# Kernel optimization log

Hardware: AMD Instinct MI355X
Metric: run time of the kernel (lower is better)

The kernel has to match this reference:

```python
import jax, jax.numpy as jnp
import numpy as np

B, N, C = 4, 2048, 64   # batch, tokens, num_feat
HS = 512                # hidden_size
H = HS // C             # 8 heads, head_dim = C = 64
EPS = 1e-6


def _ln(x, g, b):
    m = x.mean(-1, keepdims=True)
    v = ((x - m) ** 2).mean(-1, keepdims=True)
    return (x - m) / jnp.sqrt(v + EPS) * g + b


def setup_inputs() -> dict:
    key = jax.random.key(0)
    ks = jax.random.split(key, 8)
    s = 0.02
    return {
        "x": jax.random.normal(ks[0], (B, N, C), jnp.float32),
        "g1": jnp.ones((C,), jnp.float32),
        "be1": jnp.zeros((C,), jnp.float32),
        "Wqkv": jax.random.normal(ks[1], (C, 3 * HS), jnp.float32) * s,
        "bqkv": jnp.zeros((3 * HS,), jnp.float32),
        "Wout": jax.random.normal(ks[2], (HS, C), jnp.float32) * s,
        "bout": jnp.zeros((C,), jnp.float32),
        "g2": jnp.ones((C,), jnp.float32),
        "be2": jnp.zeros((C,), jnp.float32),
        "W1": jax.random.normal(ks[3], (C, HS // 8), jnp.float32) * s,
        "b1": jax.random.normal(ks[4], (HS // 8,), jnp.float32) * 1e-6,
        "W2": jax.random.normal(ks[5], (HS // 8, C), jnp.float32) * s,
        "b2": jax.random.normal(ks[6], (C,), jnp.float32) * 1e-6,
    }


def reference(x, g1, be1, Wqkv, bqkv, Wout, bout, g2, be2, W1, b1, W2, b2):
    b_, n_, c_ = x.shape
    hs = Wout.shape[0]
    h_ = hs // c_
    res = x
    y = _ln(x, g1, be1)
    # fused QKV: (B,N,3*HS) -> (3,B,H,N,D) with D = c_
    qkv = (y @ Wqkv + bqkv).reshape(b_, n_, 3, h_, c_).transpose(2, 0, 3, 1, 4)
    q, k, v = qkv[0], qkv[1], qkv[2]
    scores = jnp.einsum('bhqd,bhkd->bhqk', q, k) / jnp.sqrt(jnp.asarray(c_, x.dtype))
    probs = jax.nn.softmax(scores, axis=-1)
    ctx = jnp.einsum('bhqk,bhkd->bhqd', probs, v)
    ctx = ctx.transpose(0, 2, 1, 3).reshape(b_, n_, hs)
    attn = jax.nn.gelu(ctx @ Wout + bout, approximate=False)  # GELU after out proj per source
    x2 = attn + res
    y2 = _ln(x2, g2, be2)
    mlp = jax.nn.gelu(y2 @ W1 + b1, approximate=False) @ W2 + b2
    return mlp + x2
```

## Files before the change

### kernel.cpp

```cpp
#include <hip/hip_runtime.h>


#define NN 2048
#define CC 64
#define HH 8
#define HSZ 512

typedef __bf16 bf16x8 __attribute__((ext_vector_type(8)));
typedef float f32x4 __attribute__((ext_vector_type(4)));

__device__ __forceinline__ float b2f(unsigned short u) {
  union { unsigned int i; float f; } v; v.i = ((unsigned int)u) << 16; return v.f;
}
__device__ __forceinline__ unsigned short f2b(float f) {
  union { float f; unsigned int i; } v; v.f = f;
  unsigned int r = v.i + 0x7FFFu + ((v.i >> 16) & 1u);
  return (unsigned short)(r >> 16);
}
__device__ __forceinline__ unsigned int pk2(float a, float b) {
  return (unsigned int)f2b(a) | ((unsigned int)f2b(b) << 16);
}
__device__ __forceinline__ unsigned char f2fp8(float f) {
  int p = __builtin_amdgcn_cvt_pk_fp8_f32(f, f, 0, false);
  return (unsigned char)(p & 0xFF);
}
__device__ __forceinline__ float gelu_f(float x) {
  return 0.5f * x * (1.0f + erff(x * 0.7071067811865475f));
}

__global__ __launch_bounds__(256) void k_ln_qkv(
    const float* __restrict__ x,
    const float* __restrict__ g1,
    const float* __restrict__ be1,
    const float* __restrict__ W,
    const float* __restrict__ bqkv,
    unsigned char* __restrict__ Qb,
    unsigned char* __restrict__ Kb,
    unsigned char* __restrict__ VbT)
{
  __shared__ __align__(16) unsigned short As[64 * 72];
  __shared__ __align__(16) unsigned short Ws[128 * 72];
  const int tid = threadIdx.x, wv = tid >> 6, lane = tid & 63;
  const int col = lane & 15, quad = lane >> 4;
  const int bm = blockIdx.x & 127, bn = blockIdx.x >> 7;
  const int m0 = bm * 64, nw = bn * 128;

  const int c4 = tid & 15;
  float4 gv = *(const float4*)(g1 + c4 * 4);
  float4 bv = *(const float4*)(be1 + c4 * 4);
  #pragma unroll
  for (int s = 0; s < 4; ++s) {
    int idx = s * 256 + tid;
    int row = idx >> 4;
    float4 xv = *(const float4*)(x + (size_t)(m0 + row) * CC + c4 * 4);
    float ps = xv.x + xv.y + xv.z + xv.w;
    float ps2 = xv.x * xv.x + xv.y * xv.y + xv.z * xv.z + xv.w * xv.w;
    #pragma unroll
    for (int off = 8; off; off >>= 1) {
      ps += __shfl_xor(ps, off, 16);
      ps2 += __shfl_xor(ps2, off, 16);
    }
    float mean = ps * (1.0f / 64.0f);
    float var = ps2 * (1.0f / 64.0f) - mean * mean;
    float rs = rsqrtf(var + 1e-6f);
    uint2 packed;
    packed.x = pk2((xv.x - mean) * rs * gv.x + bv.x, (xv.y - mean) * rs * gv.y + bv.y);
    packed.y = pk2((xv.z - mean) * rs * gv.z + bv.z, (xv.w - mean) * rs * gv.w + bv.w);
    *(uint2*)&As[row * 72 + c4 * 4] = packed;
  }

  {
    const int c_loc = tid & 127;
    const int kg = tid >> 7;
    const int ng = nw + c_loc;
    #pragma unroll
    for (int g = 0; g < 4; ++g) {
      float wv8[8];
      #pragma unroll
      for (int j = 0; j < 8; ++j) wv8[j] = W[(size_t)(kg * 32 + g * 8 + j) * 1536 + ng];
      uint4 u;
      u.x = pk2(wv8[0], wv8[1]); u.y = pk2(wv8[2], wv8[3]);
      u.z = pk2(wv8[4], wv8[5]); u.w = pk2(wv8[6], wv8[7]);
      *(uint4*)&Ws[c_loc * 72 + kg * 32 + g * 8] = u;
    }
  }
  __syncthreads();

  bf16x8 af0 = *(const bf16x8*)&As[(wv * 16 + col) * 72 + quad * 8];
  bf16x8 af1 = *(const bf16x8*)&As[(wv * 16 + col) * 72 + 32 + quad * 8];

  f32x4 acc[8];
  #pragma unroll
  for (int nt = 0; nt < 8; ++nt) acc[nt] = (f32x4){0.f, 0.f, 0.f, 0.f};
  #pragma unroll
  for (int nt = 0; nt < 8; ++nt) {
    bf16x8 b0 = *(const bf16x8*)&Ws[(nt * 16 + col) * 72 + quad * 8];
    bf16x8 b1 = *(const bf16x8*)&Ws[(nt * 16 + col) * 72 + 32 + quad * 8];
    acc[nt] = __builtin_amdgcn_mfma_f32_16x16x32_bf16(af0, b0, acc[nt], 0, 0, 0);
    acc[nt] = __builtin_amdgcn_mfma_f32_16x16x32_bf16(af1, b1, acc[nt], 0, 0, 0);
  }

  const int tkb = m0 + wv * 16 + quad * 4;
  const int bb = tkb >> 11;
  const int nnb = tkb & 2047;
  #pragma unroll
  for (int nt = 0; nt < 8; ++nt) {
    const int n0 = nw + nt * 16;
    const int which = n0 >> 9;
    const int h = (n0 >> 6) & 7;
    const int d0 = n0 & 63;
    const float bias = bqkv[n0 + col];
    float vv[4];
    #pragma unroll
    for (int r = 0; r < 4; ++r) vv[r] = acc[nt][r] + bias;
    if (which == 2) {
      int lo = __builtin_amdgcn_cvt_pk_fp8_f32(vv[0], vv[1], 0, false);
      int full = __builtin_amdgcn_cvt_pk_fp8_f32(vv[2], vv[3], lo, true);
      *(unsigned int*)(VbT + ((size_t)(bb * HH + h) * CC + d0 + col) * NN + nnb) =
          (unsigned int)full;
    } else {
      unsigned char* dst = (which == 0) ? Qb : Kb;
      #pragma unroll
      for (int r = 0; r < 4; ++r)
        dst[((size_t)(bb * HH + h) * NN + nnb + r) * CC + d0 + col] = f2fp8(vv[r]);
    }
  }
}

__global__ __launch_bounds__(256) void k_attn(
    const unsigned char* __restrict__ Q,
    const unsigned char* __restrict__ K,
    const unsigned char* __restrict__ VT,
    const float* __restrict__ Wout,
    unsigned short* __restrict__ part)
{
  __shared__ __align__(16) unsigned char smem[18432];
  unsigned char* Ks = smem;
  unsigned char* Vt = smem + 5120;
  unsigned char* Ps = smem + 10240;
  unsigned short* Wb = (unsigned short*)smem;
  unsigned short* Ob = (unsigned short*)(smem + 9216);
  const int tid = threadIdx.x, wv = tid >> 6, lane = tid & 63;
  const int col = lane & 15, quad = lane >> 4;
  const int bh = blockIdx.x >> 5, qc = blockIdx.x & 31;
  const size_t base = (size_t)bh * NN * CC;
  const int q0 = qc * 64 + wv * 16;

  long qf0 = *(const long*)(Q + base + (size_t)(q0 + col) * CC + quad * 8);
  long qf1 = *(const long*)(Q + base + (size_t)(q0 + col) * CC + 32 + quad * 8);

  f32x4 o[4];
  float lsum[4] = {0.f, 0.f, 0.f, 0.f};
  #pragma unroll
  for (int dt = 0; dt < 4; ++dt) o[dt] = (f32x4){0.f, 0.f, 0.f, 0.f};
  unsigned char* Pw = Ps + wv * (16 * 80);

  for (int kt = 0; kt < 32; ++kt) {
    const int kb = kt * 64;
    {
      int row = tid >> 2, c16 = (tid & 3) << 4;
      *(uint4*)&Ks[row * 80 + c16] = *(const uint4*)(K + base + (size_t)(kb + row) * CC + c16);
      *(uint4*)&Vt[row * 80 + c16] = *(const uint4*)(VT + base + (size_t)row * NN + kb + c16);
    }
    __syncthreads();

    #pragma unroll
    for (int ct = 0; ct < 4; ++ct) {
      long k0 = *(const long*)&Ks[(ct * 16 + col) * 80 + quad * 8];
      long k1 = *(const long*)&Ks[(ct * 16 + col) * 80 + 32 + quad * 8];
      f32x4 a = (f32x4){0.f, 0.f, 0.f, 0.f};
      a = __builtin_amdgcn_mfma_f32_16x16x32_fp8_fp8(qf0, k0, a, 0, 0, 0);
      a = __builtin_amdgcn_mfma_f32_16x16x32_fp8_fp8(qf1, k1, a, 0, 0, 0);
      #pragma unroll
      for (int r = 0; r < 4; ++r) {
        float pv = __expf(a[r] * 0.125f);
        lsum[r] += pv;
        Pw[(quad * 4 + r) * 80 + ct * 16 + col] = f2fp8(pv);
      }
    }
    long pa0 = *(const long*)&Pw[col * 80 + quad * 8];
    long pa1 = *(const long*)&Pw[col * 80 + 32 + quad * 8];
    #pragma unroll
    for (int dt = 0; dt < 4; ++dt) {
      long v0 = *(const long*)&Vt[(dt * 16 + col) * 80 + quad * 8];
      long v1 = *(const long*)&Vt[(dt * 16 + col) * 80 + 32 + quad * 8];
      o[dt] = __builtin_amdgcn_mfma_f32_16x16x32_fp8_fp8(pa0, v0, o[dt], 0, 0, 0);
      o[dt] = __builtin_amdgcn_mfma_f32_16x16x32_fp8_fp8(pa1, v1, o[dt], 0, 0, 0);
    }
    __syncthreads();
  }

  #pragma unroll
  for (int r = 0; r < 4; ++r) {
    float v = lsum[r];
    #pragma unroll
    for (int off = 8; off; off >>= 1) v += __shfl_xor(v, off, 16);
    float inv = 1.0f / v;
    #pragma unroll
    for (int dt = 0; dt < 4; ++dt) o[dt][r] *= inv;
  }

  const int h = bh & 7, b = bh >> 3;
  {
    const int c = tid & 63, kg = tid >> 6;
    #pragma unroll
    for (int j = 0; j < 16; ++j)
      Wb[c * 72 + kg * 16 + j] = f2b(Wout[(size_t)(h * 64 + kg * 16 + j) * 64 + c]);
  }
  unsigned short* Obw = Ob + wv * (16 * 72);
  #pragma unroll
  for (int dt = 0; dt < 4; ++dt)
    #pragma unroll
    for (int r = 0; r < 4; ++r)
      Obw[(quad * 4 + r) * 72 + dt * 16 + col] = f2b(o[dt][r]);
  __syncthreads();

  bf16x8 oa0 = *(const bf16x8*)&Obw[col * 72 + quad * 8];
  bf16x8 oa1 = *(const bf16x8*)&Obw[col * 72 + 32 + quad * 8];
  #pragma unroll
  for (int nt = 0; nt < 4; ++nt) {
    bf16x8 bw0 = *(const bf16x8*)&Wb[(nt * 16 + col) * 72 + quad * 8];
    bf16x8 bw1 = *(const bf16x8*)&Wb[(nt * 16 + col) * 72 + 32 + quad * 8];
    f32x4 ac = (f32x4){0.f, 0.f, 0.f, 0.f};
    ac = __builtin_amdgcn_mfma_f32_16x16x32_bf16(oa0, bw0, ac, 0, 0, 0);
    ac = __builtin_amdgcn_mfma_f32_16x16x32_bf16(oa1, bw1, ac, 0, 0, 0);
    #pragma unroll
    for (int r = 0; r < 4; ++r) {
      int n = q0 + quad * 4 + r;
      part[((size_t)(b * HH + h) * NN + n) * CC + nt * 16 + col] = f2b(ac[r]);
    }
  }
}

__global__ __launch_bounds__(256) void k_post(
    const unsigned short* __restrict__ part,
    const float* __restrict__ x,
    const float* __restrict__ bout,
    const float* __restrict__ g2,
    const float* __restrict__ be2,
    const float* __restrict__ W1,
    const float* __restrict__ b1,
    const float* __restrict__ W2,
    const float* __restrict__ b2v,
    float* __restrict__ out)
{
  __shared__ __align__(16) float Ws1[64 * 64];
  __shared__ __align__(16) float Ws2[64 * 64];
  __shared__ float ys[4][64], hs[4][64];
  const int tid = threadIdx.x, wid = tid >> 6, lane = tid & 63;
  const int tk = blockIdx.x * 4 + wid;
  const int b = tk >> 11, n = tk & 2047;

  #pragma unroll
  for (int p = 0; p < 4; ++p) {
    int idx = p * 256 + tid;
    *(float4*)&Ws1[idx * 4] = *(const float4*)(W1 + idx * 4);
    *(float4*)&Ws2[idx * 4] = *(const float4*)(W2 + idx * 4);
  }

  float proj = 0.f;
  #pragma unroll
  for (int h = 0; h < 8; ++h)
    proj += b2f(part[((size_t)(b * HH + h) * NN + n) * CC + lane]);

  float a = gelu_f(proj + bout[lane]);
  float x2 = a + x[(size_t)tk * CC + lane];
  float s = x2;
  #pragma unroll
  for (int off = 32; off; off >>= 1) s += __shfl_xor(s, off, 64);
  float mean = s * (1.0f / 64.0f);
  float d = x2 - mean;
  float vs = d * d;
  #pragma unroll
  for (int off = 32; off; off >>= 1) vs += __shfl_xor(vs, off, 64);
  float var = vs * (1.0f / 64.0f);
  ys[wid][lane] = d * rsqrtf(var + 1e-6f) * g2[lane] + be2[lane];
  __syncthreads();

  float acc2 = 0.f;
  #pragma unroll 8
  for (int c = 0; c < 64; ++c) acc2 += ys[wid][c] * Ws1[c * 64 + lane];
  hs[wid][lane] = gelu_f(acc2 + b1[lane]);

  float acc3 = 0.f;
  #pragma unroll 8
  for (int c = 0; c < 64; ++c) acc3 += hs[wid][c] * Ws2[c * 64 + lane];
  out[(size_t)tk * CC + lane] = acc3 + b2v[lane] + x2;
}

extern "C" void kernel_launch(void* const* d_in, const int* in_sizes, int n_in,
                              void* d_out, int out_size, void* d_ws, size_t ws_size,
                              hipStream_t stream) {
  const float* x    = (const float*)d_in[0];
  const float* g1   = (const float*)d_in[1];
  const float* be1  = (const float*)d_in[2];
  const float* Wqkv = (const float*)d_in[3];
  const float* bqkv = (const float*)d_in[4];
  const float* Wout = (const float*)d_in[5];
  const float* bout = (const float*)d_in[6];
  const float* g2   = (const float*)d_in[7];
  const float* be2  = (const float*)d_in[8];
  const float* W1   = (const float*)d_in[9];
  const float* b1   = (const float*)d_in[10];
  const float* W2   = (const float*)d_in[11];
  const float* b2   = (const float*)d_in[12];
  float* out = (float*)d_out;

  unsigned char* wsb = (unsigned char*)d_ws;
  const size_t SZ = (size_t)4 * HH * NN * CC;
  unsigned char* Qb   = wsb;
  unsigned char* Kb   = wsb + SZ;
  unsigned char* VbT  = wsb + 2 * SZ;
  unsigned short* part = (unsigned short*)(wsb + 3 * SZ);

  k_ln_qkv<<<1536, 256, 0, stream>>>(x, g1, be1, Wqkv, bqkv, Qb, Kb, VbT);
  k_attn<<<1024, 256, 0, stream>>>(Qb, Kb, VbT, Wout, part);
  k_post<<<2048, 256, 0, stream>>>(part, x, bout, g2, be2, W1, b1, W2, b2, out);
}
```

Baseline: 170.0 us.

## Split attention keys across two blocks, keep probabilities in registers, defer normalization

The attention kernel now gives each wave two 16-row query tiles and splits the key range in half across two blocks, writing unnormalized partial projections and row sums that the post kernel combines and normalizes. The scale 1/sqrt(d)*log2(e) is folded into Q and K quantization so exp2 replaces the scaled exp. The QK MFMA operands are swapped so probabilities stay in registers and are redistributed with lane shuffles instead of going through LDS. This trades doubled partial-output traffic and extra reads in k_post for more K/V reuse per tile load, fewer LDS round trips and shorter per-block loops. Folding the scale into each of Q and K before FP8 quantization also changes their magnitudes and therefore the rounding error.

Result: faster. 163.9 us (-3.6%).

```diff
diff --git a/kernel.cpp b/kernel.cpp
--- a/kernel.cpp
+++ b/kernel.cpp
@@ -5,6 +5,7 @@
 #define CC 64
 #define HH 8
 #define HSZ 512
+#define QKSCALE 0.42466092f
 
 typedef __bf16 bf16x8 __attribute__((ext_vector_type(8)));
 typedef float f32x4 __attribute__((ext_vector_type(4)));
@@ -122,7 +123,8 @@
       unsigned char* dst = (which == 0) ? Qb : Kb;
       #pragma unroll
       for (int r = 0; r < 4; ++r)
-        dst[((size_t)(bb * HH + h) * NN + nnb + r) * CC + d0 + col] = f2fp8(vv[r]);
+        dst[((size_t)(bb * HH + h) * NN + nnb + r) * CC + d0 + col] =
+            f2fp8(vv[r] * QKSCALE);
     }
   }
 }
@@ -132,108 +134,140 @@
     const unsigned char* __restrict__ K,
     const unsigned char* __restrict__ VT,
     const float* __restrict__ Wout,
-    unsigned short* __restrict__ part)
+    unsigned short* __restrict__ part,
+    float* __restrict__ lsums)
 {
-  __shared__ __align__(16) unsigned char smem[18432];
+  __shared__ __align__(16) unsigned char smem[27648];
   unsigned char* Ks = smem;
   unsigned char* Vt = smem + 5120;
-  unsigned char* Ps = smem + 10240;
   unsigned short* Wb = (unsigned short*)smem;
   unsigned short* Ob = (unsigned short*)(smem + 9216);
   const int tid = threadIdx.x, wv = tid >> 6, lane = tid & 63;
   const int col = lane & 15, quad = lane >> 4;
-  const int bh = blockIdx.x >> 5, qc = blockIdx.x & 31;
+  const int bid = blockIdx.x;
+  const int tc = bid & 1, qc = (bid >> 1) & 15, bh = bid >> 5;
   const size_t base = (size_t)bh * NN * CC;
-  const int q0 = qc * 64 + wv * 16;
-
-  long qf0 = *(const long*)(Q + base + (size_t)(q0 + col) * CC + quad * 8);
-  long qf1 = *(const long*)(Q + base + (size_t)(q0 + col) * CC + 32 + quad * 8);
-
-  f32x4 o[4];
-  float lsum[4] = {0.f, 0.f, 0.f, 0.f};
-  #pragma unroll
-  for (int dt = 0; dt < 4; ++dt) o[dt] = (f32x4){0.f, 0.f, 0.f, 0.f};
-  unsigned char* Pw = Ps + wv * (16 * 80);
-
-  for (int kt = 0; kt < 32; ++kt) {
-    const int kb = kt * 64;
+  const int q0 = qc * 128 + wv * 32;
+  const int t0 = tc * 1024;
+
+  long qf[2][2];
+  #pragma unroll
+  for (int mt = 0; mt < 2; ++mt)
+    #pragma unroll
+    for (int kh = 0; kh < 2; ++kh)
+      qf[mt][kh] = *(const long*)(Q + base + (size_t)(q0 + mt * 16 + col) * CC + kh * 32 + quad * 8);
+
+  f32x4 o[2][4];
+  #pragma unroll
+  for (int mt = 0; mt < 2; ++mt)
+    #pragma unroll
+    for (int dt = 0; dt < 4; ++dt) o[mt][dt] = (f32x4){0.f, 0.f, 0.f, 0.f};
+  float ls[2] = {0.f, 0.f};
+  const int sl0 = ((quad & 1) << 5) + col;
+  const int sl1 = sl0 + 16;
+  const bool hiq = (quad >= 2);
+
+  for (int kt = 0; kt < 16; ++kt) {
+    const int tb = t0 + kt * 64;
     {
       int row = tid >> 2, c16 = (tid & 3) << 4;
-      *(uint4*)&Ks[row * 80 + c16] = *(const uint4*)(K + base + (size_t)(kb + row) * CC + c16);
-      *(uint4*)&Vt[row * 80 + c16] = *(const uint4*)(VT + base + (size_t)row * NN + kb + c16);
+      *(uint4*)&Ks[row * 80 + c16] = *(const uint4*)(K + base + (size_t)(tb + row) * CC + c16);
+      *(uint4*)&Vt[row * 80 + c16] = *(const uint4*)(VT + base + (size_t)row * NN + tb + c16);
     }
     __syncthreads();
 
+    unsigned int Dw[2][4];
     #pragma unroll
     for (int ct = 0; ct < 4; ++ct) {
       long k0 = *(const long*)&Ks[(ct * 16 + col) * 80 + quad * 8];
       long k1 = *(const long*)&Ks[(ct * 16 + col) * 80 + 32 + quad * 8];
-      f32x4 a = (f32x4){0.f, 0.f, 0.f, 0.f};
-      a = __builtin_amdgcn_mfma_f32_16x16x32_fp8_fp8(qf0, k0, a, 0, 0, 0);
-      a = __builtin_amdgcn_mfma_f32_16x16x32_fp8_fp8(qf1, k1, a, 0, 0, 0);
-      #pragma unroll
-      for (int r = 0; r < 4; ++r) {
-        float pv = __expf(a[r] * 0.125f);
-        lsum[r] += pv;
-        Pw[(quad * 4 + r) * 80 + ct * 16 + col] = f2fp8(pv);
+      #pragma unroll
+      for (int mt = 0; mt < 2; ++mt) {
+        f32x4 a = (f32x4){0.f, 0.f, 0.f, 0.f};
+        a = __builtin_amdgcn_mfma_f32_16x16x32_fp8_fp8(k0, qf[mt][0], a, 0, 0, 0);
+        a = __builtin_amdgcn_mfma_f32_16x16x32_fp8_fp8(k1, qf[mt][1], a, 0, 0, 0);
+        float p0 = exp2f(a[0]), p1 = exp2f(a[1]);
+        float p2 = exp2f(a[2]), p3 = exp2f(a[3]);
+        ls[mt] += (p0 + p1) + (p2 + p3);
+        int lo = __builtin_amdgcn_cvt_pk_fp8_f32(p0, p1, 0, false);
+        Dw[mt][ct] = (unsigned int)__builtin_amdgcn_cvt_pk_fp8_f32(p2, p3, lo, true);
       }
     }
-    long pa0 = *(const long*)&Pw[col * 80 + quad * 8];
-    long pa1 = *(const long*)&Pw[col * 80 + 32 + quad * 8];
-    #pragma unroll
-    for (int dt = 0; dt < 4; ++dt) {
-      long v0 = *(const long*)&Vt[(dt * 16 + col) * 80 + quad * 8];
-      long v1 = *(const long*)&Vt[(dt * 16 + col) * 80 + 32 + quad * 8];
-      o[dt] = __builtin_amdgcn_mfma_f32_16x16x32_fp8_fp8(pa0, v0, o[dt], 0, 0, 0);
-      o[dt] = __builtin_amdgcn_mfma_f32_16x16x32_fp8_fp8(pa1, v1, o[dt], 0, 0, 0);
+
+    #pragma unroll
+    for (int kh = 0; kh < 2; ++kh) {
+      long pb[2];
+      #pragma unroll
+      for (int mt = 0; mt < 2; ++mt) {
+        unsigned int a0 = (unsigned int)__shfl((int)Dw[mt][2 * kh], sl0, 64);
+        unsigned int b0 = (unsigned int)__shfl((int)Dw[mt][2 * kh + 1], sl0, 64);
+        unsigned int a1 = (unsigned int)__shfl((int)Dw[mt][2 * kh], sl1, 64);
+        unsigned int b1 = (unsigned int)__shfl((int)Dw[mt][2 * kh + 1], sl1, 64);
+        unsigned long lo = hiq ? b0 : a0;
+        unsigned long hi = hiq ? b1 : a1;
+        pb[mt] = (long)(lo | (hi << 32));
+      }
+      #pragma unroll
+      for (int dt = 0; dt < 4; ++dt) {
+        long vf = *(const long*)&Vt[(dt * 16 + col) * 80 + kh * 32 + quad * 8];
+        o[0][dt] = __builtin_amdgcn_mfma_f32_16x16x32_fp8_fp8(vf, pb[0], o[0][dt], 0, 0, 0);
+        o[1][dt] = __builtin_amdgcn_mfma_f32_16x16x32_fp8_fp8(vf, pb[1], o[1][dt], 0, 0, 0);
+      }
     }
     __syncthreads();
   }
 
-  #pragma unroll
-  for (int r = 0; r < 4; ++r) {
-    float v = lsum[r];
-    #pragma unroll
-    for (int off = 8; off; off >>= 1) v += __shfl_xor(v, off, 16);
-    float inv = 1.0f / v;
-    #pragma unroll
-    for (int dt = 0; dt < 4; ++dt) o[dt][r] *= inv;
-  }
-
   const int h = bh & 7, b = bh >> 3;
+  #pragma unroll
+  for (int mt = 0; mt < 2; ++mt) {
+    float v = ls[mt];
+    v += __shfl_xor(v, 16, 64);
+    v += __shfl_xor(v, 32, 64);
+    if (quad == 0)
+      lsums[(size_t)(tc * 32 + bh) * NN + q0 + mt * 16 + col] = v;
+  }
+
   {
     const int c = tid & 63, kg = tid >> 6;
     #pragma unroll
     for (int j = 0; j < 16; ++j)
       Wb[c * 72 + kg * 16 + j] = f2b(Wout[(size_t)(h * 64 + kg * 16 + j) * 64 + c]);
   }
-  unsigned short* Obw = Ob + wv * (16 * 72);
-  #pragma unroll
-  for (int dt = 0; dt < 4; ++dt)
-    #pragma unroll
-    for (int r = 0; r < 4; ++r)
-      Obw[(quad * 4 + r) * 72 + dt * 16 + col] = f2b(o[dt][r]);
+  unsigned short* Obw = Ob + wv * (32 * 72);
+  #pragma unroll
+  for (int mt = 0; mt < 2; ++mt)
+    #pragma unroll
+    for (int dt = 0; dt < 4; ++dt) {
+      uint2 u;
+      u.x = pk2(o[mt][dt][0], o[mt][dt][1]);
+      u.y = pk2(o[mt][dt][2], o[mt][dt][3]);
+      *(uint2*)&Obw[(mt * 16 + col) * 72 + dt * 16 + quad * 4] = u;
+    }
   __syncthreads();
 
-  bf16x8 oa0 = *(const bf16x8*)&Obw[col * 72 + quad * 8];
-  bf16x8 oa1 = *(const bf16x8*)&Obw[col * 72 + 32 + quad * 8];
-  #pragma unroll
-  for (int nt = 0; nt < 4; ++nt) {
-    bf16x8 bw0 = *(const bf16x8*)&Wb[(nt * 16 + col) * 72 + quad * 8];
-    bf16x8 bw1 = *(const bf16x8*)&Wb[(nt * 16 + col) * 72 + 32 + quad * 8];
-    f32x4 ac = (f32x4){0.f, 0.f, 0.f, 0.f};
-    ac = __builtin_amdgcn_mfma_f32_16x16x32_bf16(oa0, bw0, ac, 0, 0, 0);
-    ac = __builtin_amdgcn_mfma_f32_16x16x32_bf16(oa1, bw1, ac, 0, 0, 0);
-    #pragma unroll
-    for (int r = 0; r < 4; ++r) {
-      int n = q0 + quad * 4 + r;
-      part[((size_t)(b * HH + h) * NN + n) * CC + nt * 16 + col] = f2b(ac[r]);
+  #pragma unroll
+  for (int mt = 0; mt < 2; ++mt) {
+    bf16x8 oa0 = *(const bf16x8*)&Obw[(mt * 16 + col) * 72 + quad * 8];
+    bf16x8 oa1 = *(const bf16x8*)&Obw[(mt * 16 + col) * 72 + 32 + quad * 8];
+    #pragma unroll
+    for (int nt = 0; nt < 4; ++nt) {
+      bf16x8 bw0 = *(const bf16x8*)&Wb[(nt * 16 + col) * 72 + quad * 8];
+      bf16x8 bw1 = *(const bf16x8*)&Wb[(nt * 16 + col) * 72 + 32 + quad * 8];
+      f32x4 ac = (f32x4){0.f, 0.f, 0.f, 0.f};
+      ac = __builtin_amdgcn_mfma_f32_16x16x32_bf16(oa0, bw0, ac, 0, 0, 0);
+      ac = __builtin_amdgcn_mfma_f32_16x16x32_bf16(oa1, bw1, ac, 0, 0, 0);
+      #pragma unroll
+      for (int r = 0; r < 4; ++r) {
+        int n = q0 + mt * 16 + quad * 4 + r;
+        part[((size_t)(tc * 32 + bh) * NN + n) * CC + nt * 16 + col] = f2b(ac[r]);
+      }
     }
   }
 }
 
 __global__ __launch_bounds__(256) void k_post(
     const unsigned short* __restrict__ part,
+    const float* __restrict__ lsums,
     const float* __restrict__ x,
     const float* __restrict__ bout,
     const float* __restrict__ g2,
@@ -260,8 +294,13 @@
 
   float proj = 0.f;
   #pragma unroll
-  for (int h = 0; h < 8; ++h)
-    proj += b2f(part[((size_t)(b * HH + h) * NN + n) * CC + lane]);
+  for (int h = 0; h < 8; ++h) {
+    size_t i0 = (size_t)(b * HH + h) * NN + n;
+    size_t i1 = i0 + (size_t)32 * NN;
+    float p = b2f(part[i0 * CC + lane]) + b2f(part[i1 * CC + lane]);
+    float l = lsums[i0] + lsums[i1];
+    proj += p * __builtin_amdgcn_rcpf(l);
+  }
 
   float a = gelu_f(proj + bout[lane]);
   float x2 = a + x[(size_t)tk * CC + lane];
@@ -312,8 +351,9 @@
   unsigned char* Kb   = wsb + SZ;
   unsigned char* VbT  = wsb + 2 * SZ;
   unsigned short* part = (unsigned short*)(wsb + 3 * SZ);
+  float* lsums         = (float*)(wsb + 3 * SZ + 4 * SZ);
 
   k_ln_qkv<<<1536, 256, 0, stream>>>(x, g1, be1, Wqkv, bqkv, Qb, Kb, VbT);
-  k_attn<<<1024, 256, 0, stream>>>(Qb, Kb, VbT, Wout, part);
-  k_post<<<2048, 256, 0, stream>>>(part, x, bout, g2, be2, W1, b1, W2, b2, out);
-}
+  k_attn<<<1024, 256, 0, stream>>>(Qb, Kb, VbT, Wout, part, lsums);
+  k_post<<<2048, 256, 0, stream>>>(part, lsums, x, bout, g2, be2, W1, b1, W2, b2, out);
+}
```
